# Optimization experiments

Hardware: AMD Instinct MI355X
Metric: run time of the kernel (lower is better)

Reference implementation:

```python
import jax, jax.numpy as jnp
import numpy as np

B, C_HIGH, C_LOW, H, W = 4, 256, 128, 64, 64
HEADS = 4
HEAD_DIM = C_LOW // HEADS
FFN = 2 * C_LOW
EPS = 1e-5


def group_norm1(x, w, b):
    # GroupNorm(num_groups=1): normalize over (C,H,W) per sample, per-channel affine
    mu = jnp.mean(x, axis=(1, 2, 3), keepdims=True)
    var = jnp.var(x, axis=(1, 2, 3), keepdims=True)
    xn = (x - mu) * jax.lax.rsqrt(var + EPS)
    return xn * w[None, :, None, None] + b[None, :, None, None]


def conv1x1(x, Wm):
    # 1x1 conv, no bias: Wm [C_out, C_in], x [B,C_in,H,W]
    return jnp.einsum('oc,bchw->bohw', Wm, x)


def setup_inputs() -> dict:
    key = jax.random.key(0)
    ks = jax.random.split(key, 10)
    s = 0.05
    return {
        'high_feature': jax.random.normal(ks[0], (B, C_HIGH, H, W), jnp.float32),
        'low_feature': jax.random.normal(ks[1], (B, C_LOW, H, W), jnp.float32),
        'norm_high_w': jnp.ones((C_HIGH,), jnp.float32),
        'norm_high_b': jnp.zeros((C_HIGH,), jnp.float32),
        'norm_low_w': jnp.ones((C_LOW,), jnp.float32),
        'norm_low_b': jnp.zeros((C_LOW,), jnp.float32),
        'norm_ffn_w': jnp.ones((C_LOW,), jnp.float32),
        'norm_ffn_b': jnp.zeros((C_LOW,), jnp.float32),
        'Wq': jax.random.normal(ks[2], (C_LOW, C_HIGH), jnp.float32) * s,
        'Wk': jax.random.normal(ks[3], (C_LOW, C_LOW), jnp.float32) * s,
        'Wv': jax.random.normal(ks[4], (C_LOW, C_LOW), jnp.float32) * s,
        'Wproj': jax.random.normal(ks[5], (C_LOW, C_LOW), jnp.float32) * s,
        'Wffn1': jax.random.normal(ks[6], (FFN, C_LOW), jnp.float32) * s,
        'Wffn2': jax.random.normal(ks[7], (C_LOW, FFN), jnp.float32) * s,
        # nn.Parameter(torch.zeros(1)) in the original; use 0.1 for nontrivial grads
        'gamma_attn': jnp.full((1,), 0.1, jnp.float32),
        'gamma_ffn': jnp.full((1,), 0.1, jnp.float32),
    }


def reference(high_feature, low_feature, norm_high_w, norm_high_b, norm_low_w,
              norm_low_b, norm_ffn_w, norm_ffn_b, Wq, Wk, Wv, Wproj, Wffn1,
              Wffn2, gamma_attn, gamma_ffn):
    Bb, _, Hh, Ww = low_feature.shape
    N = Hh * Ww
    scale = HEAD_DIM ** (-0.5)

    high_norm = group_norm1(high_feature, norm_high_w, norm_high_b)
    low_norm = group_norm1(low_feature, norm_low_w, norm_low_b)

    q = conv1x1(high_norm, Wq).reshape(Bb, HEADS, HEAD_DIM, N).transpose(0, 1, 3, 2)  # [B,h,N,d]
    k = conv1x1(low_norm, Wk).reshape(Bb, HEADS, HEAD_DIM, N)                         # [B,h,d,N]
    v = conv1x1(low_norm, Wv).reshape(Bb, HEADS, HEAD_DIM, N).transpose(0, 1, 3, 2)   # [B,h,N,d]

    attn = jax.nn.softmax(jnp.einsum('bhnd,bhdm->bhnm', q, k) * scale, axis=-1)       # [B,h,N,N]
    out = jnp.einsum('bhnm,bhmd->bhnd', attn, v)                                      # [B,h,N,d]
    out = out.transpose(0, 1, 3, 2).reshape(Bb, C_LOW, Hh, Ww)
    out = conv1x1(out, Wproj)

    x = low_feature + gamma_attn[0] * out
    xn = group_norm1(x, norm_ffn_w, norm_ffn_b)
    ffn = conv1x1(jax.nn.gelu(conv1x1(xn, Wffn1), approximate=False), Wffn2)
    return x + gamma_ffn[0] * ffn
```

## Files before the change

kernel.cpp:

```cpp
#include <hip/hip_runtime.h>
#include <hip/hip_bf16.h>
#include <math.h>

#define EPS 1e-5f
#define BB 4
#define CHIGH 256
#define CLOW 128
#define NN 4096
#define NHEADS 4
#define HDIM 32
#define FFN_DIM 256

typedef __bf16 b8 __attribute__((ext_vector_type(8)));
typedef float f4 __attribute__((ext_vector_type(4)));

__device__ __forceinline__ unsigned int cvt_pk(float lo, float hi) {
    float2 t; t.x = lo; t.y = hi;
    __hip_bfloat162 h = __float22bfloat162_rn(t);
    unsigned int r;
    __builtin_memcpy(&r, &h, sizeof(r));
    return r;
}

__global__ __launch_bounds__(256)
void stats_kernel(const float* __restrict__ X, float* __restrict__ acc, int perSample)
{
    const int b = blockIdx.y;
    const float4* xp = (const float4*)(X + (size_t)b * perSample);
    const int n4 = perSample >> 2;
    float s = 0.f, s2 = 0.f;
    for (int i = blockIdx.x * blockDim.x + threadIdx.x; i < n4; i += gridDim.x * blockDim.x) {
        float4 v = xp[i];
        s  += v.x + v.y + v.z + v.w;
        s2 += v.x * v.x + v.y * v.y + v.z * v.z + v.w * v.w;
    }
    for (int off = 32; off; off >>= 1) {
        s  += __shfl_down(s, off, 64);
        s2 += __shfl_down(s2, off, 64);
    }
    __shared__ float ls[4], ls2[4];
    const int w = threadIdx.x >> 6;
    if ((threadIdx.x & 63) == 0) { ls[w] = s; ls2[w] = s2; }
    __syncthreads();
    if (threadIdx.x == 0) {
        atomicAdd(&acc[2 * b], ls[0] + ls[1] + ls[2] + ls[3]);
        atomicAdd(&acc[2 * b + 1], ls2[0] + ls2[1] + ls2[2] + ls2[3]);
    }
}

template<int MODE, int M, int K, int NORM_X, int COMBINE, int OUT_T, int STATS>
__global__ __launch_bounds__(256)
void mfma_gemm(const float* __restrict__ Wm, const float* __restrict__ X,
               void* __restrict__ Yv, const float* __restrict__ R,
               const float* __restrict__ gp, const float* __restrict__ nw,
               const float* __restrict__ nb, const float* __restrict__ st,
               const float* __restrict__ Lp, float* __restrict__ stOut,
               float oscale)
{
    constexpr int KP = K + 8;
    __shared__ unsigned short Ws[M][KP];
    __shared__ unsigned short Xs[64][40];
    __shared__ float red[8];
    const int b = blockIdx.y;
    const int n0 = blockIdx.x * 64;
    const int t = threadIdx.x;
    const int w = t >> 6, lm = t & 15, quad = (t & 63) >> 4;

    float mean = 0.f, rstd = 0.f;
    if (NORM_X) {
        const float invCnt = 1.0f / ((float)K * NN);
        mean = st[2 * b] * invCnt;
        const float var = st[2 * b + 1] * invCnt - mean * mean;
        rstd = rsqrtf(var + EPS);
    }

    const float* Xb = X + (size_t)b * K * NN;
    const int k2 = (t & 15) * 2;
    const int nc = (t >> 4) * 4;

    float4 pa, pb, pc_, pd_, pl0, pl1;
    float w0 = 0.f, w1 = 0.f, c0 = 0.f, c1 = 0.f;

    auto fetch = [&](int kc) {
        const size_t ro = (size_t)(kc + k2) * NN + n0 + nc;
        pa = *(const float4*)&Xb[ro];
        pb = *(const float4*)&Xb[ro + NN];
        if (COMBINE) {
            pc_ = *(const float4*)&Xb[ro + (size_t)BB * CLOW * NN];
            pd_ = *(const float4*)&Xb[ro + (size_t)BB * CLOW * NN + NN];
            const int hh = (kc + k2) >> 5;
            const size_t lo = (size_t)(b * NHEADS + hh) * NN + n0 + nc;
            pl0 = *(const float4*)&Lp[lo];
            pl1 = *(const float4*)&Lp[lo + (size_t)BB * NHEADS * NN];
        }
        if (NORM_X) {
            w0 = nw[kc + k2]; w1 = nw[kc + k2 + 1];
            c0 = nb[kc + k2]; c1 = nb[kc + k2 + 1];
        }
    };

    auto stage = [&]() {
        float4 xa = pa, xb = pb;
        if (COMBINE) {
            const float i0 = 1.f / (pl0.x + pl1.x), i1 = 1.f / (pl0.y + pl1.y);
            const float i2 = 1.f / (pl0.z + pl1.z), i3 = 1.f / (pl0.w + pl1.w);
            xa.x = (pa.x + pc_.x) * i0; xa.y = (pa.y + pc_.y) * i1;
            xa.z = (pa.z + pc_.z) * i2; xa.w = (pa.w + pc_.w) * i3;
            xb.x = (pb.x + pd_.x) * i0; xb.y = (pb.y + pd_.y) * i1;
            xb.z = (pb.z + pd_.z) * i2; xb.w = (pb.w + pd_.w) * i3;
        } else if (NORM_X) {
            const float sc0 = w0 * rstd, sb0 = c0 - mean * sc0;
            const float sc1 = w1 * rstd, sb1 = c1 - mean * sc1;
            xa.x = pa.x * sc0 + sb0; xa.y = pa.y * sc0 + sb0;
            xa.z = pa.z * sc0 + sb0; xa.w = pa.w * sc0 + sb0;
            xb.x = pb.x * sc1 + sb1; xb.y = pb.y * sc1 + sb1;
            xb.z = pb.z * sc1 + sb1; xb.w = pb.w * sc1 + sb1;
        }
        unsigned int* xw = (unsigned int*)&Xs[0][0];
        xw[(nc + 0) * 20 + (t & 15)] = cvt_pk(xa.x, xb.x);
        xw[(nc + 1) * 20 + (t & 15)] = cvt_pk(xa.y, xb.y);
        xw[(nc + 2) * 20 + (t & 15)] = cvt_pk(xa.z, xb.z);
        xw[(nc + 3) * 20 + (t & 15)] = cvt_pk(xa.w, xb.w);
    };

    fetch(0);

    for (int idx = t * 8; idx < M * K; idx += 256 * 8) {
        const int r_ = idx / K;
        const int cc = idx & (K - 1);
        float4 wa = *(const float4*)&Wm[idx];
        float4 wb = *(const float4*)&Wm[idx + 4];
        uint4 pk;
        pk.x = cvt_pk(wa.x, wa.y); pk.y = cvt_pk(wa.z, wa.w);
        pk.z = cvt_pk(wb.x, wb.y); pk.w = cvt_pk(wb.z, wb.w);
        *(uint4*)&Ws[r_][cc] = pk;
    }

    f4 acc[M / 16];
    #pragma unroll
    for (int f = 0; f < M / 16; f++) acc[f] = (f4){0.f, 0.f, 0.f, 0.f};

    #pragma unroll
    for (int kc = 0; kc < K; kc += 32) {
        if (kc) __syncthreads();
        stage();
        __syncthreads();
        if (kc + 32 < K) fetch(kc + 32);
        b8 bx = *(const b8*)&Xs[w * 16 + lm][quad * 8];
        #pragma unroll
        for (int f = 0; f < M / 16; f++) {
            b8 af = *(const b8*)&Ws[f * 16 + lm][kc + quad * 8];
            acc[f] = __builtin_amdgcn_mfma_f32_16x16x32_bf16(af, bx, acc[f], 0, 0, 0);
        }
    }

    if (OUT_T) {
        unsigned short* Yt = (unsigned short*)Yv;
        #pragma unroll
        for (int f = 0; f < M / 16; f++) {
            const int hh = f >> 1;
            const int ddb = (f & 1) * 16 + quad * 4;
            uint2 pk;
            pk.x = cvt_pk(acc[f][0] * oscale, acc[f][1] * oscale);
            pk.y = cvt_pk(acc[f][2] * oscale, acc[f][3] * oscale);
            const size_t off = ((size_t)(b * NHEADS + hh) * NN + n0 + w * 16 + lm) * 32 + ddb;
            *(uint2*)&Yt[off] = pk;
        }
    } else {
        float* Yb = (float*)Yv + (size_t)b * M * NN;
        const float g = (MODE == 2) ? gp[0] : 0.f;
        const float* Rb = (MODE == 2) ? (R + (size_t)b * M * NN) : nullptr;
        float s = 0.f, s2 = 0.f;
        #pragma unroll
        for (int f = 0; f < M / 16; f++)
            #pragma unroll
            for (int r = 0; r < 4; r++) {
                const size_t off = (size_t)(f * 16 + quad * 4 + r) * NN + n0 + w * 16 + lm;
                float v = acc[f][r];
                if (MODE == 1) v = 0.5f * v * (1.f + erff(v * 0.70710678118654752f));
                if (MODE == 2) v = Rb[off] + g * v;
                Yb[off] = v;
                if (STATS) { s += v; s2 += v * v; }
            }
        if (STATS) {
            for (int off = 32; off; off >>= 1) {
                s  += __shfl_down(s, off, 64);
                s2 += __shfl_down(s2, off, 64);
            }
            if ((t & 63) == 0) { red[w] = s; red[4 + w] = s2; }
            __syncthreads();
            if (t == 0) {
                atomicAdd(&stOut[2 * b], red[0] + red[1] + red[2] + red[3]);
                atomicAdd(&stOut[2 * b + 1], red[4] + red[5] + red[6] + red[7]);
            }
        }
    }
}

__global__ __launch_bounds__(256)
void flash_kernel(const unsigned short* __restrict__ Qt,
                  const unsigned short* __restrict__ Kt,
                  const float* __restrict__ Vm,
                  float* __restrict__ Op, float* __restrict__ Lp)
{
    __shared__ unsigned short Vst[32][72];
    __shared__ unsigned short Ps[4][32][72];

    const int bz = blockIdx.z;
    const int b = bz >> 1, half = bz & 1;
    const int h = blockIdx.y;
    const int n0 = blockIdx.x * 128;
    const int t = threadIdx.x;
    const int w = t >> 6;
    const int lm = t & 15, quad = (t & 63) >> 4;

    const unsigned short* Qh = Qt + (size_t)(b * NHEADS + h) * NN * 32;
    const unsigned short* Kh = Kt + (size_t)(b * NHEADS + h) * NN * 32;
    const float* Vh = Vm + ((size_t)b * CLOW + h * HDIM) * NN;

    b8 aq[2];
    aq[0] = *(const b8*)&Qh[(size_t)(n0 + w * 32 + lm) * 32 + quad * 8];
    aq[1] = *(const b8*)&Qh[(size_t)(n0 + w * 32 + 16 + lm) * 32 + quad * 8];

    b8 ones;
    #pragma unroll
    for (int j = 0; j < 8; j++) ones[j] = (__bf16)1.0f;

    f4 ocT[2][2];
    f4 lsum[2];
    #pragma unroll
    for (int u = 0; u < 2; u++) {
        lsum[u] = (f4){0.f, 0.f, 0.f, 0.f};
        ocT[0][u] = (f4){0.f, 0.f, 0.f, 0.f};
        ocT[1][u] = (f4){0.f, 0.f, 0.f, 0.f};
    }

    const int m_lo = half * (NN / 2), m_hi = m_lo + NN / 2;
    for (int m0 = m_lo; m0 < m_hi; m0 += 64) {
        b8 bk[4];
        #pragma unroll
        for (int f = 0; f < 4; f++)
            bk[f] = *(const b8*)&Kh[(size_t)(m0 + f * 16 + lm) * 32 + quad * 8];

        __syncthreads();
        {
            const int d = t >> 3;
            const int mc = (t & 7) * 8;
            const float* vp = Vh + (size_t)d * NN + m0 + mc;
            float4 va = *(const float4*)vp, vb = *(const float4*)(vp + 4);
            uint4 pv;
            pv.x = cvt_pk(va.x, va.y); pv.y = cvt_pk(va.z, va.w);
            pv.z = cvt_pk(vb.x, vb.y); pv.w = cvt_pk(vb.z, vb.w);
            *(uint4*)&Vst[d][mc] = pv;
        }
        __syncthreads();

        f4 st[4][2];
        #pragma unroll
        for (int f = 0; f < 4; f++)
            #pragma unroll
            for (int u = 0; u < 2; u++) {
                f4 z = {0.f, 0.f, 0.f, 0.f};
                st[f][u] = __builtin_amdgcn_mfma_f32_16x16x32_bf16(bk[f], aq[u], z, 0, 0, 0);
            }

        #pragma unroll
        for (int f = 0; f < 4; f++)
            #pragma unroll
            for (int u = 0; u < 2; u++) {
                float e0 = __expf(st[f][u][0]);
                float e1 = __expf(st[f][u][1]);
                float e2 = __expf(st[f][u][2]);
                float e3 = __expf(st[f][u][3]);
                uint2 pk;
                pk.x = cvt_pk(e0, e1);
                pk.y = cvt_pk(e2, e3);
                *(uint2*)&Ps[w][u * 16 + lm][f * 16 + quad * 4] = pk;
            }

        #pragma unroll
        for (int c = 0; c < 2; c++) {
            b8 av0 = *(const b8*)&Vst[lm][c * 32 + quad * 8];
            b8 av1 = *(const b8*)&Vst[16 + lm][c * 32 + quad * 8];
            #pragma unroll
            for (int u = 0; u < 2; u++) {
                b8 bp = *(const b8*)&Ps[w][u * 16 + lm][c * 32 + quad * 8];
                ocT[0][u] = __builtin_amdgcn_mfma_f32_16x16x32_bf16(av0, bp, ocT[0][u], 0, 0, 0);
                ocT[1][u] = __builtin_amdgcn_mfma_f32_16x16x32_bf16(av1, bp, ocT[1][u], 0, 0, 0);
                lsum[u]   = __builtin_amdgcn_mfma_f32_16x16x32_bf16(ones, bp, lsum[u], 0, 0, 0);
            }
        }
    }

    float* OpB = Op + ((size_t)(half * BB + b) * CLOW + h * HDIM) * NN;
    float* LpB = Lp + ((size_t)(half * BB + b) * NHEADS + h) * NN;
    #pragma unroll
    for (int u = 0; u < 2; u++) {
        const int n = n0 + w * 32 + u * 16 + lm;
        if (quad == 0) LpB[n] = lsum[u][0];
        #pragma unroll
        for (int hh = 0; hh < 2; hh++)
            #pragma unroll
            for (int r = 0; r < 4; r++) {
                const int d = hh * 16 + quad * 4 + r;
                OpB[(size_t)d * NN + n] = ocT[hh][u][r];
            }
    }
}

extern "C" void kernel_launch(void* const* d_in, const int* in_sizes, int n_in,
                              void* d_out, int out_size, void* d_ws, size_t ws_size,
                              hipStream_t stream)
{
    const float* high  = (const float*)d_in[0];
    const float* low   = (const float*)d_in[1];
    const float* nh_w  = (const float*)d_in[2];
    const float* nh_b  = (const float*)d_in[3];
    const float* nl_w  = (const float*)d_in[4];
    const float* nl_b  = (const float*)d_in[5];
    const float* nf_w  = (const float*)d_in[6];
    const float* nf_b  = (const float*)d_in[7];
    const float* Wq    = (const float*)d_in[8];
    const float* Wk    = (const float*)d_in[9];
    const float* Wv    = (const float*)d_in[10];
    const float* Wproj = (const float*)d_in[11];
    const float* Wff1  = (const float*)d_in[12];
    const float* Wff2  = (const float*)d_in[13];
    const float* g_at  = (const float*)d_in[14];
    const float* g_ff  = (const float*)d_in[15];
    float* out = (float*)d_out;

    float* ws    = (float*)d_ws;
    float* stats = ws;
    unsigned short* qt = (unsigned short*)(ws + 64);
    unsigned short* kt = qt + (size_t)BB * NHEADS * NN * 32;
    float* vv    = (float*)(kt + (size_t)BB * NHEADS * NN * 32);
    float* opart = vv + (size_t)BB * CLOW * NN;
    float* lpart = opart + (size_t)2 * BB * CLOW * NN;
    float* x     = lpart + (size_t)2 * BB * NHEADS * NN;
    float* hbuf  = x + (size_t)BB * CLOW * NN;

    (void)hipMemsetAsync(stats, 0, 64 * sizeof(float), stream);

    stats_kernel<<<dim3(64, BB), 256, 0, stream>>>(high, stats + 0, CHIGH * NN);
    stats_kernel<<<dim3(64, BB), 256, 0, stream>>>(low,  stats + 8, CLOW * NN);

    mfma_gemm<0, CLOW, CHIGH, 1, 0, 1, 0><<<dim3(64, BB), 256, 0, stream>>>(
        Wq, high, qt, nullptr, nullptr, nh_w, nh_b, stats + 0, nullptr, nullptr,
        0.17677669529663687f);
    mfma_gemm<0, CLOW, CLOW, 1, 0, 1, 0><<<dim3(64, BB), 256, 0, stream>>>(
        Wk, low, kt, nullptr, nullptr, nl_w, nl_b, stats + 8, nullptr, nullptr, 1.0f);
    mfma_gemm<0, CLOW, CLOW, 1, 0, 0, 0><<<dim3(64, BB), 256, 0, stream>>>(
        Wv, low, vv, nullptr, nullptr, nl_w, nl_b, stats + 8, nullptr, nullptr, 1.0f);

    flash_kernel<<<dim3(NN / 128, NHEADS, BB * 2), 256, 0, stream>>>(qt, kt, vv,
                                                                     opart, lpart);

    mfma_gemm<2, CLOW, CLOW, 0, 1, 0, 1><<<dim3(64, BB), 256, 0, stream>>>(
        Wproj, opart, x, low, g_at, nullptr, nullptr, nullptr, lpart, stats + 16, 1.0f);

    mfma_gemm<1, FFN_DIM, CLOW, 1, 0, 0, 0><<<dim3(64, BB), 256, 0, stream>>>(
        Wff1, x, hbuf, nullptr, nullptr, nf_w, nf_b, stats + 16, nullptr, nullptr, 1.0f);
    mfma_gemm<2, CLOW, FFN_DIM, 0, 0, 0, 0><<<dim3(64, BB), 256, 0, stream>>>(
        Wff2, hbuf, out, x, g_ff, nullptr, nullptr, nullptr, nullptr, nullptr, 1.0f);
}
```

Baseline: 262.6 us.

## Pre-convert weights to bf16, restructure GEMM tiles, store V as bf16

A new kernel converts all six weight matrices to bf16 once per call. The GEMMs then read their A-fragments straight from global bf16 instead of staging converted fp32 weights in LDS. Each GEMM block now covers 32 columns with the M dimension split across warps, loads the whole K-slab of X into LDS at once, and launches twice as many blocks. The V projection writes bf16, so the flash kernel loads V fragments directly from global memory and skips its per-tile LDS staging and two barriers. The trade-off is uncoalesced global fragment loads in place of LDS reuse, plus an extra kernel launch.

```diff
diff --git a/kernel.cpp b/kernel.cpp
--- a/kernel.cpp
+++ b/kernel.cpp
@@ -48,23 +48,44 @@
     }
 }
 
+__global__ __launch_bounds__(256)
+void wconv_kernel(const float* __restrict__ w0, const float* __restrict__ w1,
+                  const float* __restrict__ w2, const float* __restrict__ w3,
+                  const float* __restrict__ w4, const float* __restrict__ w5,
+                  unsigned short* __restrict__ dst)
+{
+    const int m = blockIdx.y;
+    const int sizes[6] = {32768, 16384, 16384, 16384, 32768, 32768};
+    const int offs[6]  = {0, 32768, 49152, 65536, 81920, 114688};
+    const float* src = m == 0 ? w0 : m == 1 ? w1 : m == 2 ? w2 : m == 3 ? w3
+                     : m == 4 ? w4 : w5;
+    const int i = (blockIdx.x * 256 + threadIdx.x) * 4;
+    if (i >= sizes[m]) return;
+    float4 v = *(const float4*)&src[i];
+    uint2 pk;
+    pk.x = cvt_pk(v.x, v.y);
+    pk.y = cvt_pk(v.z, v.w);
+    *(uint2*)&dst[offs[m] + i] = pk;
+}
+
 template<int MODE, int M, int K, int NORM_X, int COMBINE, int OUT_T, int STATS>
 __global__ __launch_bounds__(256)
-void mfma_gemm(const float* __restrict__ Wm, const float* __restrict__ X,
+void mfma_gemm(const unsigned short* __restrict__ Wb, const float* __restrict__ X,
                void* __restrict__ Yv, const float* __restrict__ R,
                const float* __restrict__ gp, const float* __restrict__ nw,
                const float* __restrict__ nb, const float* __restrict__ st,
                const float* __restrict__ Lp, float* __restrict__ stOut,
                float oscale)
 {
-    constexpr int KP = K + 8;
-    __shared__ unsigned short Ws[M][KP];
-    __shared__ unsigned short Xs[64][40];
+    constexpr int MH = M / 2;
+    constexpr int KP2 = (K + 8) / 2;
+    __shared__ unsigned short Xs[32][K + 8];
     __shared__ float red[8];
     const int b = blockIdx.y;
-    const int n0 = blockIdx.x * 64;
+    const int n0 = blockIdx.x * 32;
     const int t = threadIdx.x;
     const int w = t >> 6, lm = t & 15, quad = (t & 63) >> 4;
+    const int ng = w & 1, mh = w >> 1;
 
     float mean = 0.f, rstd = 0.f;
     if (NORM_X) {
@@ -75,107 +96,93 @@
     }
 
     const float* Xb = X + (size_t)b * K * NN;
-    const int k2 = (t & 15) * 2;
-    const int nc = (t >> 4) * 4;
-
-    float4 pa, pb, pc_, pd_, pl0, pl1;
-    float w0 = 0.f, w1 = 0.f, c0 = 0.f, c1 = 0.f;
-
-    auto fetch = [&](int kc) {
-        const size_t ro = (size_t)(kc + k2) * NN + n0 + nc;
-        pa = *(const float4*)&Xb[ro];
-        pb = *(const float4*)&Xb[ro + NN];
+    unsigned int* xw = (unsigned int*)&Xs[0][0];
+
+    #pragma unroll
+    for (int it = 0; it < K / 64; it++) {
+        const int s = it * 256 + t;
+        const int kp = s >> 3;
+        const int k2 = kp << 1;
+        const int nc = (s & 7) << 2;
+        const size_t ro = (size_t)k2 * NN + n0 + nc;
+        float4 pa = *(const float4*)&Xb[ro];
+        float4 pb = *(const float4*)&Xb[ro + NN];
         if (COMBINE) {
-            pc_ = *(const float4*)&Xb[ro + (size_t)BB * CLOW * NN];
-            pd_ = *(const float4*)&Xb[ro + (size_t)BB * CLOW * NN + NN];
-            const int hh = (kc + k2) >> 5;
+            float4 pc_ = *(const float4*)&Xb[ro + (size_t)BB * CLOW * NN];
+            float4 pd_ = *(const float4*)&Xb[ro + (size_t)BB * CLOW * NN + NN];
+            const int hh = k2 >> 5;
             const size_t lo = (size_t)(b * NHEADS + hh) * NN + n0 + nc;
-            pl0 = *(const float4*)&Lp[lo];
-            pl1 = *(const float4*)&Lp[lo + (size_t)BB * NHEADS * NN];
-        }
-        if (NORM_X) {
-            w0 = nw[kc + k2]; w1 = nw[kc + k2 + 1];
-            c0 = nb[kc + k2]; c1 = nb[kc + k2 + 1];
-        }
-    };
-
-    auto stage = [&]() {
-        float4 xa = pa, xb = pb;
-        if (COMBINE) {
+            float4 pl0 = *(const float4*)&Lp[lo];
+            float4 pl1 = *(const float4*)&Lp[lo + (size_t)BB * NHEADS * NN];
             const float i0 = 1.f / (pl0.x + pl1.x), i1 = 1.f / (pl0.y + pl1.y);
             const float i2 = 1.f / (pl0.z + pl1.z), i3 = 1.f / (pl0.w + pl1.w);
-            xa.x = (pa.x + pc_.x) * i0; xa.y = (pa.y + pc_.y) * i1;
-            xa.z = (pa.z + pc_.z) * i2; xa.w = (pa.w + pc_.w) * i3;
-            xb.x = (pb.x + pd_.x) * i0; xb.y = (pb.y + pd_.y) * i1;
-            xb.z = (pb.z + pd_.z) * i2; xb.w = (pb.w + pd_.w) * i3;
+            pa.x = (pa.x + pc_.x) * i0; pa.y = (pa.y + pc_.y) * i1;
+            pa.z = (pa.z + pc_.z) * i2; pa.w = (pa.w + pc_.w) * i3;
+            pb.x = (pb.x + pd_.x) * i0; pb.y = (pb.y + pd_.y) * i1;
+            pb.z = (pb.z + pd_.z) * i2; pb.w = (pb.w + pd_.w) * i3;
         } else if (NORM_X) {
-            const float sc0 = w0 * rstd, sb0 = c0 - mean * sc0;
-            const float sc1 = w1 * rstd, sb1 = c1 - mean * sc1;
-            xa.x = pa.x * sc0 + sb0; xa.y = pa.y * sc0 + sb0;
-            xa.z = pa.z * sc0 + sb0; xa.w = pa.w * sc0 + sb0;
-            xb.x = pb.x * sc1 + sb1; xb.y = pb.y * sc1 + sb1;
-            xb.z = pb.z * sc1 + sb1; xb.w = pb.w * sc1 + sb1;
-        }
-        unsigned int* xw = (unsigned int*)&Xs[0][0];
-        xw[(nc + 0) * 20 + (t & 15)] = cvt_pk(xa.x, xb.x);
-        xw[(nc + 1) * 20 + (t & 15)] = cvt_pk(xa.y, xb.y);
-        xw[(nc + 2) * 20 + (t & 15)] = cvt_pk(xa.z, xb.z);
-        xw[(nc + 3) * 20 + (t & 15)] = cvt_pk(xa.w, xb.w);
-    };
-
-    fetch(0);
-
-    for (int idx = t * 8; idx < M * K; idx += 256 * 8) {
-        const int r_ = idx / K;
-        const int cc = idx & (K - 1);
-        float4 wa = *(const float4*)&Wm[idx];
-        float4 wb = *(const float4*)&Wm[idx + 4];
-        uint4 pk;
-        pk.x = cvt_pk(wa.x, wa.y); pk.y = cvt_pk(wa.z, wa.w);
-        pk.z = cvt_pk(wb.x, wb.y); pk.w = cvt_pk(wb.z, wb.w);
-        *(uint4*)&Ws[r_][cc] = pk;
-    }
-
-    f4 acc[M / 16];
-    #pragma unroll
-    for (int f = 0; f < M / 16; f++) acc[f] = (f4){0.f, 0.f, 0.f, 0.f};
+            const float sc0 = nw[k2] * rstd,     sb0 = nb[k2] - mean * sc0;
+            const float sc1 = nw[k2 + 1] * rstd, sb1 = nb[k2 + 1] - mean * sc1;
+            pa.x = pa.x * sc0 + sb0; pa.y = pa.y * sc0 + sb0;
+            pa.z = pa.z * sc0 + sb0; pa.w = pa.w * sc0 + sb0;
+            pb.x = pb.x * sc1 + sb1; pb.y = pb.y * sc1 + sb1;
+            pb.z = pb.z * sc1 + sb1; pb.w = pb.w * sc1 + sb1;
+        }
+        xw[(nc + 0) * KP2 + kp] = cvt_pk(pa.x, pb.x);
+        xw[(nc + 1) * KP2 + kp] = cvt_pk(pa.y, pb.y);
+        xw[(nc + 2) * KP2 + kp] = cvt_pk(pa.z, pb.z);
+        xw[(nc + 3) * KP2 + kp] = cvt_pk(pa.w, pb.w);
+    }
+    __syncthreads();
+
+    f4 acc[MH / 16];
+    #pragma unroll
+    for (int f = 0; f < MH / 16; f++) acc[f] = (f4){0.f, 0.f, 0.f, 0.f};
 
     #pragma unroll
     for (int kc = 0; kc < K; kc += 32) {
-        if (kc) __syncthreads();
-        stage();
-        __syncthreads();
-        if (kc + 32 < K) fetch(kc + 32);
-        b8 bx = *(const b8*)&Xs[w * 16 + lm][quad * 8];
-        #pragma unroll
-        for (int f = 0; f < M / 16; f++) {
-            b8 af = *(const b8*)&Ws[f * 16 + lm][kc + quad * 8];
+        b8 bx = *(const b8*)&Xs[ng * 16 + lm][kc + quad * 8];
+        #pragma unroll
+        for (int f = 0; f < MH / 16; f++) {
+            b8 af = *(const b8*)&Wb[(size_t)(mh * MH + f * 16 + lm) * K + kc + quad * 8];
             acc[f] = __builtin_amdgcn_mfma_f32_16x16x32_bf16(af, bx, acc[f], 0, 0, 0);
         }
     }
 
-    if (OUT_T) {
+    const int n = n0 + ng * 16 + lm;
+    if (OUT_T == 1) {
         unsigned short* Yt = (unsigned short*)Yv;
         #pragma unroll
-        for (int f = 0; f < M / 16; f++) {
-            const int hh = f >> 1;
-            const int ddb = (f & 1) * 16 + quad * 4;
+        for (int f = 0; f < MH / 16; f++) {
+            const int mb = mh * MH + f * 16 + quad * 4;
+            const int hh = mb >> 5, ddb = mb & 31;
             uint2 pk;
             pk.x = cvt_pk(acc[f][0] * oscale, acc[f][1] * oscale);
             pk.y = cvt_pk(acc[f][2] * oscale, acc[f][3] * oscale);
-            const size_t off = ((size_t)(b * NHEADS + hh) * NN + n0 + w * 16 + lm) * 32 + ddb;
-            *(uint2*)&Yt[off] = pk;
-        }
+            *(uint2*)&Yt[((size_t)(b * NHEADS + hh) * NN + n) * 32 + ddb] = pk;
+        }
+    } else if (OUT_T == 2) {
+        unsigned short* Yt = (unsigned short*)Yv + (size_t)b * M * NN;
+        #pragma unroll
+        for (int f = 0; f < MH / 16; f++)
+            #pragma unroll
+            for (int r = 0; r < 4; r++) {
+                const int m = mh * MH + f * 16 + quad * 4 + r;
+                float v = acc[f][r];
+                unsigned int u = cvt_pk(v, v);
+                Yt[(size_t)m * NN + n] = (unsigned short)(u & 0xFFFF);
+            }
     } else {
         float* Yb = (float*)Yv + (size_t)b * M * NN;
         const float g = (MODE == 2) ? gp[0] : 0.f;
         const float* Rb = (MODE == 2) ? (R + (size_t)b * M * NN) : nullptr;
         float s = 0.f, s2 = 0.f;
         #pragma unroll
-        for (int f = 0; f < M / 16; f++)
+        for (int f = 0; f < MH / 16; f++)
             #pragma unroll
             for (int r = 0; r < 4; r++) {
-                const size_t off = (size_t)(f * 16 + quad * 4 + r) * NN + n0 + w * 16 + lm;
+                const int m = mh * MH + f * 16 + quad * 4 + r;
+                const size_t off = (size_t)m * NN + n;
                 float v = acc[f][r];
                 if (MODE == 1) v = 0.5f * v * (1.f + erff(v * 0.70710678118654752f));
                 if (MODE == 2) v = Rb[off] + g * v;
@@ -200,10 +207,9 @@
 __global__ __launch_bounds__(256)
 void flash_kernel(const unsigned short* __restrict__ Qt,
                   const unsigned short* __restrict__ Kt,
-                  const float* __restrict__ Vm,
+                  const unsigned short* __restrict__ Vt,
                   float* __restrict__ Op, float* __restrict__ Lp)
 {
-    __shared__ unsigned short Vst[32][72];
     __shared__ unsigned short Ps[4][32][72];
 
     const int bz = blockIdx.z;
@@ -216,7 +222,7 @@
 
     const unsigned short* Qh = Qt + (size_t)(b * NHEADS + h) * NN * 32;
     const unsigned short* Kh = Kt + (size_t)(b * NHEADS + h) * NN * 32;
-    const float* Vh = Vm + ((size_t)b * CLOW + h * HDIM) * NN;
+    const unsigned short* Vh = Vt + ((size_t)b * CLOW + h * HDIM) * NN;
 
     b8 aq[2];
     aq[0] = *(const b8*)&Qh[(size_t)(n0 + w * 32 + lm) * 32 + quad * 8];
@@ -237,23 +243,15 @@
 
     const int m_lo = half * (NN / 2), m_hi = m_lo + NN / 2;
     for (int m0 = m_lo; m0 < m_hi; m0 += 64) {
-        b8 bk[4];
+        b8 bk[4], av[2][2];
         #pragma unroll
         for (int f = 0; f < 4; f++)
             bk[f] = *(const b8*)&Kh[(size_t)(m0 + f * 16 + lm) * 32 + quad * 8];
-
-        __syncthreads();
-        {
-            const int d = t >> 3;
-            const int mc = (t & 7) * 8;
-            const float* vp = Vh + (size_t)d * NN + m0 + mc;
-            float4 va = *(const float4*)vp, vb = *(const float4*)(vp + 4);
-            uint4 pv;
-            pv.x = cvt_pk(va.x, va.y); pv.y = cvt_pk(va.z, va.w);
-            pv.z = cvt_pk(vb.x, vb.y); pv.w = cvt_pk(vb.z, vb.w);
-            *(uint4*)&Vst[d][mc] = pv;
-        }
-        __syncthreads();
+        #pragma unroll
+        for (int c = 0; c < 2; c++) {
+            av[0][c] = *(const b8*)&Vh[(size_t)lm * NN + m0 + c * 32 + quad * 8];
+            av[1][c] = *(const b8*)&Vh[(size_t)(16 + lm) * NN + m0 + c * 32 + quad * 8];
+        }
 
         f4 st[4][2];
         #pragma unroll
@@ -279,17 +277,14 @@
             }
 
         #pragma unroll
-        for (int c = 0; c < 2; c++) {
-            b8 av0 = *(const b8*)&Vst[lm][c * 32 + quad * 8];
-            b8 av1 = *(const b8*)&Vst[16 + lm][c * 32 + quad * 8];
+        for (int c = 0; c < 2; c++)
             #pragma unroll
             for (int u = 0; u < 2; u++) {
                 b8 bp = *(const b8*)&Ps[w][u * 16 + lm][c * 32 + quad * 8];
-                ocT[0][u] = __builtin_amdgcn_mfma_f32_16x16x32_bf16(av0, bp, ocT[0][u], 0, 0, 0);
-                ocT[1][u] = __builtin_amdgcn_mfma_f32_16x16x32_bf16(av1, bp, ocT[1][u], 0, 0, 0);
+                ocT[0][u] = __builtin_amdgcn_mfma_f32_16x16x32_bf16(av[0][c], bp, ocT[0][u], 0, 0, 0);
+                ocT[1][u] = __builtin_amdgcn_mfma_f32_16x16x32_bf16(av[1][c], bp, ocT[1][u], 0, 0, 0);
                 lsum[u]   = __builtin_amdgcn_mfma_f32_16x16x32_bf16(ones, bp, lsum[u], 0, 0, 0);
             }
-        }
     }
 
     float* OpB = Op + ((size_t)(half * BB + b) * CLOW + h * HDIM) * NN;
@@ -332,10 +327,11 @@
 
     float* ws    = (float*)d_ws;
     float* stats = ws;
-    unsigned short* qt = (unsigned short*)(ws + 64);
+    unsigned short* wbf = (unsigned short*)(ws + 64);
+    unsigned short* qt = wbf + 147456;
     unsigned short* kt = qt + (size_t)BB * NHEADS * NN * 32;
-    float* vv    = (float*)(kt + (size_t)BB * NHEADS * NN * 32);
-    float* opart = vv + (size_t)BB * CLOW * NN;
+    unsigned short* vt = kt + (size_t)BB * NHEADS * NN * 32;
+    float* opart = (float*)(vt + (size_t)BB * CLOW * NN);
     float* lpart = opart + (size_t)2 * BB * CLOW * NN;
     float* x     = lpart + (size_t)2 * BB * NHEADS * NN;
     float* hbuf  = x + (size_t)BB * CLOW * NN;
@@ -344,23 +340,24 @@
 
     stats_kernel<<<dim3(64, BB), 256, 0, stream>>>(high, stats + 0, CHIGH * NN);
     stats_kernel<<<dim3(64, BB), 256, 0, stream>>>(low,  stats + 8, CLOW * NN);
-
-    mfma_gemm<0, CLOW, CHIGH, 1, 0, 1, 0><<<dim3(64, BB), 256, 0, stream>>>(
-        Wq, high, qt, nullptr, nullptr, nh_w, nh_b, stats + 0, nullptr, nullptr,
+    wconv_kernel<<<dim3(32, 6), 256, 0, stream>>>(Wq, Wk, Wv, Wproj, Wff1, Wff2, wbf);
+
+    mfma_gemm<0, CLOW, CHIGH, 1, 0, 1, 0><<<dim3(128, BB), 256, 0, stream>>>(
+        wbf + 0, high, qt, nullptr, nullptr, nh_w, nh_b, stats + 0, nullptr, nullptr,
         0.17677669529663687f);
-    mfma_gemm<0, CLOW, CLOW, 1, 0, 1, 0><<<dim3(64, BB), 256, 0, stream>>>(
-        Wk, low, kt, nullptr, nullptr, nl_w, nl_b, stats + 8, nullptr, nullptr, 1.0f);
-    mfma_gemm<0, CLOW, CLOW, 1, 0, 0, 0><<<dim3(64, BB), 256, 0, stream>>>(
-        Wv, low, vv, nullptr, nullptr, nl_w, nl_b, stats + 8, nullptr, nullptr, 1.0f);
-
-    flash_kernel<<<dim3(NN / 128, NHEADS, BB * 2), 256, 0, stream>>>(qt, kt, vv,
+    mfma_gemm<0, CLOW, CLOW, 1, 0, 1, 0><<<dim3(128, BB), 256, 0, stream>>>(
+        wbf + 32768, low, kt, nullptr, nullptr, nl_w, nl_b, stats + 8, nullptr, nullptr, 1.0f);
+    mfma_gemm<0, CLOW, CLOW, 1, 0, 2, 0><<<dim3(128, BB), 256, 0, stream>>>(
+        wbf + 49152, low, vt, nullptr, nullptr, nl_w, nl_b, stats + 8, nullptr, nullptr, 1.0f);
+
+    flash_kernel<<<dim3(NN / 128, NHEADS, BB * 2), 256, 0, stream>>>(qt, kt, vt,
                                                                      opart, lpart);
 
-    mfma_gemm<2, CLOW, CLOW, 0, 1, 0, 1><<<dim3(64, BB), 256, 0, stream>>>(
-        Wproj, opart, x, low, g_at, nullptr, nullptr, nullptr, lpart, stats + 16, 1.0f);
-
-    mfma_gemm<1, FFN_DIM, CLOW, 1, 0, 0, 0><<<dim3(64, BB), 256, 0, stream>>>(
-        Wff1, x, hbuf, nullptr, nullptr, nf_w, nf_b, stats + 16, nullptr, nullptr, 1.0f);
-    mfma_gemm<2, CLOW, FFN_DIM, 0, 0, 0, 0><<<dim3(64, BB), 256, 0, stream>>>(
-        Wff2, hbuf, out, x, g_ff, nullptr, nullptr, nullptr, nullptr, nullptr, 1.0f);
-}
+    mfma_gemm<2, CLOW, CLOW, 0, 1, 0, 1><<<dim3(128, BB), 256, 0, stream>>>(
+        wbf + 65536, opart, x, low, g_at, nullptr, nullptr, nullptr, lpart, stats + 16, 1.0f);
+
+    mfma_gemm<1, FFN_DIM, CLOW, 1, 0, 0, 0><<<dim3(128, BB), 256, 0, stream>>>(
+        wbf + 81920, x, hbuf, nullptr, nullptr, nf_w, nf_b, stats + 16, nullptr, nullptr, 1.0f);
+    mfma_gemm<2, CLOW, FFN_DIM, 0, 0, 0, 0><<<dim3(128, BB), 256, 0, stream>>>(
+        wbf + 114688, hbuf, out, x, g_ff, nullptr, nullptr, nullptr, nullptr, nullptr, 1.0f);
+}
```

After: 287.9 us. 1.1x slower.
